# Performance work log

Measured on AMD Instinct MI355X. Metric: run time of the kernel, lower is better.

## Reference

```python
import jax, jax.numpy as jnp
import numpy as np

D_MODEL = 1024
NUM_HEADS = 16
D_K = D_MODEL // NUM_HEADS
B, S = 4, 2048


def setup_inputs() -> dict:
    key = jax.random.key(0)
    ks = jax.random.split(key, 12)
    Q = jax.random.normal(ks[0], (B, S, D_MODEL), dtype=jnp.float32)
    K = jax.random.normal(ks[1], (B, S, D_MODEL), dtype=jnp.float32)
    V = jax.random.normal(ks[2], (B, S, D_MODEL), dtype=jnp.float32)
    # causal mask: 1 where attention allowed, 0 where blocked
    mask = jnp.tril(jnp.ones((S, S), dtype=jnp.int32))[None, None, :, :]
    sc = 1.0 / np.sqrt(D_MODEL)
    Wq = jax.random.normal(ks[3], (D_MODEL, D_MODEL), dtype=jnp.float32) * sc
    Wk = jax.random.normal(ks[4], (D_MODEL, D_MODEL), dtype=jnp.float32) * sc
    Wv = jax.random.normal(ks[5], (D_MODEL, D_MODEL), dtype=jnp.float32) * sc
    Wo = jax.random.normal(ks[6], (D_MODEL, D_MODEL), dtype=jnp.float32) * sc
    bq = jnp.zeros((D_MODEL,), dtype=jnp.float32)
    bk = jnp.zeros((D_MODEL,), dtype=jnp.float32)
    bv = jnp.zeros((D_MODEL,), dtype=jnp.float32)
    bo = jnp.zeros((D_MODEL,), dtype=jnp.float32)
    return {"Q": Q, "K": K, "V": V, "mask": mask,
            "Wq": Wq, "bq": bq, "Wk": Wk, "bk": bk,
            "Wv": Wv, "bv": bv, "Wo": Wo, "bo": bo}


def reference(Q, K, V, mask, Wq, bq, Wk, bk, Wv, bv, Wo, bo):
    b = Q.shape[0]
    # projections (torch Linear: x @ W.T + b; here W stored as [in, out])
    q = Q @ Wq + bq
    k = K @ Wk + bk
    v = V @ Wv + bv
    # [B, S, D] -> [B, H, S, d_k]
    def split_heads(x):
        return x.reshape(b, -1, NUM_HEADS, D_K).transpose(0, 2, 1, 3)
    q, k, v = split_heads(q), split_heads(k), split_heads(v)
    scores = jnp.einsum('bhqd,bhkd->bhqk', q, k) / jnp.sqrt(jnp.float32(D_K))
    scores = jnp.where(mask == 0, -jnp.inf, scores)
    attn = jax.nn.softmax(scores, axis=-1)
    out = jnp.einsum('bhqk,bhkd->bhqd', attn, v)  # [B, H, S, d_k]
    out = out.transpose(0, 2, 1, 3).reshape(b, -1, NUM_HEADS * D_K)
    return out @ Wo + bo
```

## Files before the change

kernel.cpp:

```cpp
#include <hip/hip_runtime.h>

typedef __bf16 bf16_t;
typedef __bf16 bf16x8 __attribute__((ext_vector_type(8)));
typedef __bf16 bf16x4 __attribute__((ext_vector_type(4)));
typedef float  floatx4 __attribute__((ext_vector_type(4)));

#define D_MODEL 1024
#define S_LEN   2048
#define NHEAD   16
#define DK      64
#define BATCH   4
#define MROWS   (BATCH * S_LEN)
#define QSCALE  0.18033688011112042f

__device__ __forceinline__ void load_lds16(const void* gsrc, void* ldst) {
  __builtin_amdgcn_global_load_lds(
      (const __attribute__((address_space(1))) void*)gsrc,
      (__attribute__((address_space(3))) void*)ldst, 16, 0, 0);
}

__device__ __forceinline__ unsigned pack_bf16(float a, float b) {
  union { bf16_t h[2]; unsigned u; } t;
  t.h[0] = (bf16_t)a; t.h[1] = (bf16_t)b;
  return t.u;
}

__device__ __forceinline__ float bperm_f(int addr, float v) {
  union { float f; int i; } in, out;
  in.f = v;
  out.i = __builtin_amdgcn_ds_bpermute(addr, in.i);
  return out.f;
}

__global__ __launch_bounds__(256)
void transpose_w_kernel(const float* __restrict__ W0, const float* __restrict__ W1,
                        const float* __restrict__ W2, const float* __restrict__ W3,
                        bf16_t* __restrict__ T0, bf16_t* __restrict__ T1,
                        bf16_t* __restrict__ T2, bf16_t* __restrict__ T3)
{
  const int z = blockIdx.z;
  const float* W = z == 0 ? W0 : (z == 1 ? W1 : (z == 2 ? W2 : W3));
  bf16_t* Wt     = z == 0 ? T0 : (z == 1 ? T1 : (z == 2 ? T2 : T3));

  __shared__ float tile[64][65];
  const int x0 = blockIdx.x * 64;
  const int y0 = blockIdx.y * 64;
  const int tid = threadIdx.x;
  const int r = tid >> 4;
  const int c = (tid & 15) << 2;
#pragma unroll
  for (int p = 0; p < 4; p++) {
    floatx4 v = *(const floatx4*)&W[(size_t)(y0 + p * 16 + r) * D_MODEL + x0 + c];
    tile[p * 16 + r][c + 0] = v[0];
    tile[p * 16 + r][c + 1] = v[1];
    tile[p * 16 + r][c + 2] = v[2];
    tile[p * 16 + r][c + 3] = v[3];
  }
  __syncthreads();
#pragma unroll
  for (int p = 0; p < 4; p++) {
    int row = p * 16 + r;
    bf16x4 o;
    o[0] = (bf16_t)tile[c + 0][row];
    o[1] = (bf16_t)tile[c + 1][row];
    o[2] = (bf16_t)tile[c + 2][row];
    o[3] = (bf16_t)tile[c + 3][row];
    *(bf16x4*)&Wt[(size_t)(x0 + row) * D_MODEL + y0 + c] = o;
  }
}

__global__ __launch_bounds__(256, 3)
void qkv_kernel(const float* __restrict__ Qi, const float* __restrict__ Ki,
                const float* __restrict__ Vi, const bf16_t* __restrict__ Wcat,
                const float* __restrict__ bq, const float* __restrict__ bk,
                const float* __restrict__ bv,
                bf16_t* __restrict__ qo, bf16_t* __restrict__ ko,
                bf16_t* __restrict__ vo)
{
  __shared__ bf16_t As[128 * 40];
  __shared__ bf16_t Bs[128 * 32];

  const int n0g = blockIdx.x << 7;
  const int z = n0g >> 10;
  const float* A = z == 0 ? Qi : (z == 1 ? Ki : Vi);

  const int m0 = blockIdx.y << 7;
  const int tid = threadIdx.x;
  const int lane = tid & 63;
  const int w = tid >> 6;
  const int l15 = lane & 15;
  const int quad = lane >> 4;
  const int wy = (w >> 1) << 6;
  const int wx = (w & 1) << 6;
  const int w64 = w << 6;

  floatx4 acc[4][4];
#pragma unroll
  for (int i = 0; i < 4; i++)
#pragma unroll
    for (int j = 0; j < 4; j++)
#pragma unroll
      for (int r = 0; r < 4; r++) acc[i][j][r] = 0.0f;

  for (int kt = 0; kt < 32; kt++) {
    const int k0 = kt << 5;
    __syncthreads();
#pragma unroll
    for (int p = 0; p < 2; p++) {
      int slot = p * 256 + w64 + lane;
      int row = slot >> 2;
      int kc = (slot & 3) ^ (row & 3);
      load_lds16(&Wcat[(size_t)(n0g + row) * D_MODEL + k0 + (kc << 3)],
                 &Bs[(size_t)(p * 256 + w64) << 3]);
    }
#pragma unroll
    for (int p = 0; p < 4; p++) {
      int idx = p * 256 + tid;
      int r = idx >> 3, c = idx & 7;
      floatx4 v = *(const floatx4*)&A[(size_t)(m0 + r) * D_MODEL + k0 + (c << 2)];
      bf16x4 o;
      o[0] = (bf16_t)v[0]; o[1] = (bf16_t)v[1];
      o[2] = (bf16_t)v[2]; o[3] = (bf16_t)v[3];
      *(bf16x4*)&As[r * 40 + (c << 2)] = o;
    }
    __syncthreads();

    bf16x8 af[4], bfv[4];
#pragma unroll
    for (int mi = 0; mi < 4; mi++) {
      int m = wy + mi * 16 + l15;
      af[mi] = *(const bf16x8*)&As[m * 40 + (quad << 3)];
    }
#pragma unroll
    for (int ni = 0; ni < 4; ni++) {
      int n = wx + ni * 16 + l15;
      bfv[ni] = *(const bf16x8*)&Bs[n * 32 + ((quad ^ (n & 3)) << 3)];
    }
#pragma unroll
    for (int mi = 0; mi < 4; mi++)
#pragma unroll
      for (int ni = 0; ni < 4; ni++)
        acc[mi][ni] = __builtin_amdgcn_mfma_f32_16x16x32_bf16(
            af[mi], bfv[ni], acc[mi][ni], 0, 0, 0);
  }

  const float* bias = z == 0 ? bq : (z == 1 ? bk : bv);
  bf16_t* outp      = z == 0 ? qo : (z == 1 ? ko : vo);
  const float scl   = (z == 0) ? QSCALE : 1.0f;
#pragma unroll
  for (int mi = 0; mi < 4; mi++) {
#pragma unroll
    for (int ni = 0; ni < 4; ni++) {
      const int nn = (n0g + wx + ni * 16 + l15) & (D_MODEL - 1);
      const float bvv = bias[nn];
      const int h = nn >> 6, d = nn & 63;
#pragma unroll
      for (int r = 0; r < 4; r++) {
        const int m = m0 + wy + mi * 16 + quad * 4 + r;
        const int b = m >> 11, s = m & (S_LEN - 1);
        float v = (acc[mi][ni][r] + bvv) * scl;
        if (z < 2) {
          outp[((((size_t)(b * NHEAD + h) << 11) + s) << 6) + d] = (bf16_t)v;
        } else {
          outp[((((size_t)(b * NHEAD + h) << 6) + d) << 11) + s] = (bf16_t)v;
        }
      }
    }
  }
}

__global__ __launch_bounds__(256)
void out_gemm_kernel(const bf16_t* __restrict__ A, const bf16_t* __restrict__ Wt,
                     const float* __restrict__ bias, float* __restrict__ out)
{
  __shared__ bf16_t As[128 * 32];
  __shared__ bf16_t Bs[128 * 32];
  const int m0 = blockIdx.y << 7;
  const int n0 = blockIdx.x << 7;
  const int tid = threadIdx.x;
  const int lane = tid & 63;
  const int w = tid >> 6;
  const int l15 = lane & 15;
  const int quad = lane >> 4;
  const int wy = (w >> 1) << 6;
  const int wx = (w & 1) << 6;
  const int w64 = w << 6;

  floatx4 acc[4][4];
#pragma unroll
  for (int i = 0; i < 4; i++)
#pragma unroll
    for (int j = 0; j < 4; j++)
#pragma unroll
      for (int r = 0; r < 4; r++) acc[i][j][r] = 0.0f;

  for (int kt = 0; kt < 32; kt++) {
    const int k0 = kt << 5;
    __syncthreads();
#pragma unroll
    for (int p = 0; p < 2; p++) {
      int slot = p * 256 + w64 + lane;
      int row = slot >> 2;
      int kc = (slot & 3) ^ (row & 3);
      load_lds16(&A[(size_t)(m0 + row) * D_MODEL + k0 + (kc << 3)],
                 &As[(size_t)(p * 256 + w64) << 3]);
      load_lds16(&Wt[(size_t)(n0 + row) * D_MODEL + k0 + (kc << 3)],
                 &Bs[(size_t)(p * 256 + w64) << 3]);
    }
    __syncthreads();

    bf16x8 af[4], bfv[4];
#pragma unroll
    for (int mi = 0; mi < 4; mi++) {
      int m = wy + mi * 16 + l15;
      af[mi] = *(const bf16x8*)&As[m * 32 + ((quad ^ (m & 3)) << 3)];
    }
#pragma unroll
    for (int ni = 0; ni < 4; ni++) {
      int n = wx + ni * 16 + l15;
      bfv[ni] = *(const bf16x8*)&Bs[n * 32 + ((quad ^ (n & 3)) << 3)];
    }
#pragma unroll
    for (int mi = 0; mi < 4; mi++)
#pragma unroll
      for (int ni = 0; ni < 4; ni++)
        acc[mi][ni] = __builtin_amdgcn_mfma_f32_16x16x32_bf16(
            af[mi], bfv[ni], acc[mi][ni], 0, 0, 0);
  }

#pragma unroll
  for (int mi = 0; mi < 4; mi++) {
#pragma unroll
    for (int ni = 0; ni < 4; ni++) {
      const int nbase = n0 + wx + ni * 16 + l15;
      const float bv = bias[nbase];
#pragma unroll
      for (int r = 0; r < 4; r++) {
        const int m = m0 + wy + mi * 16 + quad * 4 + r;
        out[((size_t)m << 10) + nbase] = acc[mi][ni][r] + bv;
      }
    }
  }
}

__global__ __launch_bounds__(256, 4)
void attn_kernel(const bf16_t* __restrict__ qp, const bf16_t* __restrict__ kp,
                 const bf16_t* __restrict__ vtp, bf16_t* __restrict__ ob)
{
  __shared__ bf16_t Kt0[64 * 64];
  __shared__ bf16_t Kt1[64 * 64];
  __shared__ bf16_t Vt0[64 * 64];
  __shared__ bf16_t Vt1[64 * 64];

  const int pair = blockIdx.x;
  const int bh = blockIdx.y;
  const int tid = threadIdx.x;
  const int w = tid >> 6;
  const int lane = tid & 63;
  const int l15 = lane & 15;
  const int quad = lane >> 4;

  const bf16_t* Qh = qp + ((size_t)bh << 17);
  const bf16_t* Kh = kp + ((size_t)bh << 17);
  const bf16_t* Vh = vtp + ((size_t)bh << 17);
  const int b = bh >> 4, h = bh & 15;

  auto stage = [&](int k0s, bf16_t* dK, bf16_t* dV) {
#pragma unroll
    for (int p = 0; p < 2; p++) {
      const int sbase = (w << 7) + (p << 6);
      const int slot = sbase + lane;
      const int row = slot >> 3;
      const int c = (slot & 7) ^ (row & 7);
      load_lds16(&Kh[((size_t)(k0s + row) << 6) + (c << 3)], &dK[sbase << 3]);
      load_lds16(&Vh[((size_t)row << 11) + k0s + (c << 3)], &dV[sbase << 3]);
    }
  };

  int par = 0;

  auto phase = [&](int qt, bool prefetch_next_phase) {
    const int q0 = qt << 6;
    const int qbase = q0 + (w << 4);
    const int nkb = qt + 1;

    bf16x8 qf[2];
#pragma unroll
    for (int ks = 0; ks < 2; ks++)
      qf[ks] = *(const bf16x8*)&Qh[(size_t)(qbase + l15) * DK +
                                   ks * 32 + (quad << 3)];

    floatx4 acc_o[4];
    float m_i = -1e30f, l_i = 0.0f;
#pragma unroll
    for (int nd = 0; nd < 4; nd++)
#pragma unroll
      for (int r = 0; r < 4; r++) acc_o[nd][r] = 0.0f;

    for (int kb = 0; kb < nkb; kb++) {
      const int k0 = kb << 6;
      __syncthreads();

      const bf16_t* cK = par ? Kt1 : Kt0;
      const bf16_t* cV = par ? Vt1 : Vt0;
      bf16_t* nK = par ? Kt0 : Kt1;
      bf16_t* nV = par ? Vt0 : Vt1;

      if (kb + 1 < nkb)            stage((kb + 1) << 6, nK, nV);
      else if (prefetch_next_phase) stage(0, nK, nV);

      bf16x8 bk[2][4];
#pragma unroll
      for (int ks = 0; ks < 2; ks++)
#pragma unroll
        for (int ni = 0; ni < 4; ni++) {
          const int row = ni * 16 + l15;
          const int cp = ((ks << 2) + quad) ^ (row & 7);
          bk[ks][ni] = *(const bf16x8*)&cK[(row << 6) + (cp << 3)];
        }

      floatx4 st[4];
#pragma unroll
      for (int ni = 0; ni < 4; ni++)
#pragma unroll
        for (int r = 0; r < 4; r++) st[ni][r] = 0.0f;
#pragma unroll
      for (int ks = 0; ks < 2; ks++)
#pragma unroll
        for (int ni = 0; ni < 4; ni++)
          st[ni] = __builtin_amdgcn_mfma_f32_16x16x32_bf16(
              bk[ks][ni], qf[ks], st[ni], 0, 0, 0);

      if (k0 + 63 > qbase) {
        const int qrow = qbase + l15;
#pragma unroll
        for (int ni = 0; ni < 4; ni++) {
          const int keyb = k0 + ni * 16 + quad * 4;
#pragma unroll
          for (int r = 0; r < 4; r++)
            if (keyb + r > qrow) st[ni][r] = -1e30f;
        }
      }

      float v = st[0][0];
#pragma unroll
      for (int ni = 0; ni < 4; ni++)
#pragma unroll
        for (int r = 0; r < 4; r++) v = fmaxf(v, st[ni][r]);
      v = fmaxf(v, __shfl_xor(v, 16));
      v = fmaxf(v, __shfl_xor(v, 32));
      const float mn = fmaxf(m_i, v);
      const float alpha = __builtin_amdgcn_exp2f(m_i - mn);
      m_i = mn;

      unsigned pd[4][2];
      float s = 0.0f;
#pragma unroll
      for (int c = 0; c < 4; c++)
#pragma unroll
        for (int hh = 0; hh < 2; hh++) {
          float p0 = __builtin_amdgcn_exp2f(st[c][2 * hh]     - m_i);
          float p1 = __builtin_amdgcn_exp2f(st[c][2 * hh + 1] - m_i);
          s += p0 + p1;
          pd[c][hh] = pack_bf16(p0, p1);
        }
      s += __shfl_xor(s, 16);
      s += __shfl_xor(s, 32);
      l_i = l_i * alpha + s;

#pragma unroll
      for (int r = 0; r < 4; r++) {
        float ab = bperm_f((quad * 4 + r) << 2, alpha);
#pragma unroll
        for (int nd = 0; nd < 4; nd++) acc_o[nd][r] *= ab;
      }

      union AV { unsigned u[4]; bf16x8 v; };
      AV av[2];
#pragma unroll
      for (int ks = 0; ks < 2; ks++)
#pragma unroll
        for (int i = 0; i < 4; i++) {
          const int addr = ((((2 * quad + (i >> 1)) & 3) << 4) | l15) << 2;
          int lo = __builtin_amdgcn_ds_bpermute(addr, (int)pd[ks * 2][i & 1]);
          int hi = __builtin_amdgcn_ds_bpermute(addr, (int)pd[ks * 2 + 1][i & 1]);
          av[ks].u[i] = (unsigned)(quad >= 2 ? hi : lo);
        }

#pragma unroll
      for (int ks = 0; ks < 2; ks++) {
        bf16x8 bvv[4];
#pragma unroll
        for (int nd = 0; nd < 4; nd++) {
          const int row = nd * 16 + l15;
          const int cp = ((ks << 2) + quad) ^ (row & 7);
          bvv[nd] = *(const bf16x8*)&cV[(row << 6) + (cp << 3)];
        }
#pragma unroll
        for (int nd = 0; nd < 4; nd++)
          acc_o[nd] = __builtin_amdgcn_mfma_f32_16x16x32_bf16(
              av[ks].v, bvv[nd], acc_o[nd], 0, 0, 0);
      }

      par ^= 1;
    }

    const float inv = 1.0f / l_i;
#pragma unroll
    for (int r = 0; r < 4; r++) {
      const float linv = bperm_f((quad * 4 + r) << 2, inv);
      const int sRow = qbase + quad * 4 + r;
#pragma unroll
      for (int nd = 0; nd < 4; nd++) {
        const int d = nd * 16 + l15;
        ob[(((size_t)(b * S_LEN + sRow)) << 10) + h * 64 + d] =
            (bf16_t)(acc_o[nd][r] * linv);
      }
    }
  };

  stage(0, Kt0, Vt0);
  phase(31 - pair, true);
  phase(pair, false);
}

extern "C" void kernel_launch(void* const* d_in, const int* in_sizes, int n_in,
                              void* d_out, int out_size, void* d_ws, size_t ws_size,
                              hipStream_t stream)
{
  (void)in_sizes; (void)n_in; (void)out_size; (void)ws_size;
  const float* Q  = (const float*)d_in[0];
  const float* K  = (const float*)d_in[1];
  const float* V  = (const float*)d_in[2];
  const float* Wq = (const float*)d_in[4];
  const float* bq = (const float*)d_in[5];
  const float* Wk = (const float*)d_in[6];
  const float* bk = (const float*)d_in[7];
  const float* Wv = (const float*)d_in[8];
  const float* bv = (const float*)d_in[9];
  const float* Wo = (const float*)d_in[10];
  const float* bo = (const float*)d_in[11];
  float* out = (float*)d_out;

  const size_t NELT = (size_t)MROWS * D_MODEL;
  bf16_t* qp   = (bf16_t*)d_ws;
  bf16_t* kp   = qp + NELT;
  bf16_t* vtp  = kp + NELT;
  bf16_t* obuf = vtp + NELT;
  bf16_t* wqt  = obuf + NELT;
  bf16_t* wkt  = wqt + (size_t)D_MODEL * D_MODEL;
  bf16_t* wvt  = wkt + (size_t)D_MODEL * D_MODEL;
  bf16_t* wot  = wvt + (size_t)D_MODEL * D_MODEL;

  dim3 blk(256);
  transpose_w_kernel<<<dim3(16, 16, 4), blk, 0, stream>>>(
      Wq, Wk, Wv, Wo, wqt, wkt, wvt, wot);

  qkv_kernel<<<dim3(3 * D_MODEL / 128, MROWS / 128), blk, 0, stream>>>(
      Q, K, V, wqt, bq, bk, bv, qp, kp, vtp);

  attn_kernel<<<dim3(16, BATCH * NHEAD), blk, 0, stream>>>(qp, kp, vtp, obuf);

  out_gemm_kernel<<<dim3(D_MODEL / 128, MROWS / 128), blk, 0, stream>>>(
      obuf, wot, bo, out);
}
```

Baseline: 387.8 us.

## Load fp32 activations via direct-to-LDS DMA and swizzle block order for L2 reuse

```diff
diff --git a/kernel.cpp b/kernel.cpp
--- a/kernel.cpp
+++ b/kernel.cpp
@@ -77,14 +77,18 @@
                 bf16_t* __restrict__ qo, bf16_t* __restrict__ ko,
                 bf16_t* __restrict__ vo)
 {
-  __shared__ bf16_t As[128 * 40];
+  __shared__ float  Asf[128 * 32];
   __shared__ bf16_t Bs[128 * 32];
 
-  const int n0g = blockIdx.x << 7;
-  const int z = n0g >> 10;
+  const int L = blockIdx.x + 24 * blockIdx.y;
+  const int j = (L >> 3) & 7;
+  const int s = ((L >> 6) << 3) | (L & 7);
+  const int z = s >> 6;
+  const int n0g = (((z << 3) | j)) << 7;
+  const int m0 = (s & 63) << 7;
+
   const float* A = z == 0 ? Qi : (z == 1 ? Ki : Vi);
 
-  const int m0 = blockIdx.y << 7;
   const int tid = threadIdx.x;
   const int lane = tid & 63;
   const int w = tid >> 6;
@@ -98,9 +102,9 @@
 #pragma unroll
   for (int i = 0; i < 4; i++)
 #pragma unroll
-    for (int j = 0; j < 4; j++)
-#pragma unroll
-      for (int r = 0; r < 4; r++) acc[i][j][r] = 0.0f;
+    for (int jj = 0; jj < 4; jj++)
+#pragma unroll
+      for (int r = 0; r < 4; r++) acc[i][jj][r] = 0.0f;
 
   for (int kt = 0; kt < 32; kt++) {
     const int k0 = kt << 5;
@@ -115,21 +119,28 @@
     }
 #pragma unroll
     for (int p = 0; p < 4; p++) {
-      int idx = p * 256 + tid;
-      int r = idx >> 3, c = idx & 7;
-      floatx4 v = *(const floatx4*)&A[(size_t)(m0 + r) * D_MODEL + k0 + (c << 2)];
-      bf16x4 o;
-      o[0] = (bf16_t)v[0]; o[1] = (bf16_t)v[1];
-      o[2] = (bf16_t)v[2]; o[3] = (bf16_t)v[3];
-      *(bf16x4*)&As[r * 40 + (c << 2)] = o;
+      int sbase = (w << 8) + (p << 6);
+      int slot = sbase + lane;
+      int row = slot >> 3;
+      int ca = (slot & 7) ^ (row & 7);
+      load_lds16(&A[(size_t)(m0 + row) * D_MODEL + k0 + (ca << 2)],
+                 &Asf[(size_t)sbase << 2]);
     }
     __syncthreads();
 
     bf16x8 af[4], bfv[4];
 #pragma unroll
     for (int mi = 0; mi < 4; mi++) {
-      int m = wy + mi * 16 + l15;
-      af[mi] = *(const bf16x8*)&As[m * 40 + (quad << 3)];
+      const int m = wy + mi * 16 + l15;
+      const int e = m & 7;
+      floatx4 f0 = *(const floatx4*)&Asf[(m << 5) + ((((quad << 1))     ^ e) << 2)];
+      floatx4 f1 = *(const floatx4*)&Asf[(m << 5) + ((((quad << 1) | 1) ^ e) << 2)];
+      bf16x8 o;
+      o[0] = (bf16_t)f0[0]; o[1] = (bf16_t)f0[1];
+      o[2] = (bf16_t)f0[2]; o[3] = (bf16_t)f0[3];
+      o[4] = (bf16_t)f1[0]; o[5] = (bf16_t)f1[1];
+      o[6] = (bf16_t)f1[2]; o[7] = (bf16_t)f1[3];
+      af[mi] = o;
     }
 #pragma unroll
     for (int ni = 0; ni < 4; ni++) {
@@ -157,12 +168,12 @@
 #pragma unroll
       for (int r = 0; r < 4; r++) {
         const int m = m0 + wy + mi * 16 + quad * 4 + r;
-        const int b = m >> 11, s = m & (S_LEN - 1);
+        const int b = m >> 11, srow = m & (S_LEN - 1);
         float v = (acc[mi][ni][r] + bvv) * scl;
         if (z < 2) {
-          outp[((((size_t)(b * NHEAD + h) << 11) + s) << 6) + d] = (bf16_t)v;
+          outp[((((size_t)(b * NHEAD + h) << 11) + srow) << 6) + d] = (bf16_t)v;
         } else {
-          outp[((((size_t)(b * NHEAD + h) << 6) + d) << 11) + s] = (bf16_t)v;
+          outp[((((size_t)(b * NHEAD + h) << 6) + d) << 11) + srow] = (bf16_t)v;
         }
       }
     }
@@ -175,8 +186,9 @@
 {
   __shared__ bf16_t As[128 * 32];
   __shared__ bf16_t Bs[128 * 32];
-  const int m0 = blockIdx.y << 7;
-  const int n0 = blockIdx.x << 7;
+  const int L = blockIdx.x + 8 * blockIdx.y;
+  const int n0 = (((L >> 3) & 7)) << 7;
+  const int m0 = ((((L >> 6) << 3) | (L & 7))) << 7;
   const int tid = threadIdx.x;
   const int lane = tid & 63;
   const int w = tid >> 6;
@@ -190,9 +202,9 @@
 #pragma unroll
   for (int i = 0; i < 4; i++)
 #pragma unroll
-    for (int j = 0; j < 4; j++)
-#pragma unroll
-      for (int r = 0; r < 4; r++) acc[i][j][r] = 0.0f;
+    for (int jj = 0; jj < 4; jj++)
+#pragma unroll
+      for (int r = 0; r < 4; r++) acc[i][jj][r] = 0.0f;
 
   for (int kt = 0; kt < 32; kt++) {
     const int k0 = kt << 5;
@@ -306,7 +318,7 @@
       bf16_t* nK = par ? Kt0 : Kt1;
       bf16_t* nV = par ? Vt0 : Vt1;
 
-      if (kb + 1 < nkb)            stage((kb + 1) << 6, nK, nV);
+      if (kb + 1 < nkb)             stage((kb + 1) << 6, nK, nV);
       else if (prefetch_next_phase) stage(0, nK, nV);
 
       bf16x8 bk[2][4];
@@ -354,19 +366,19 @@
       m_i = mn;
 
       unsigned pd[4][2];
-      float s = 0.0f;
+      float ssum = 0.0f;
 #pragma unroll
       for (int c = 0; c < 4; c++)
 #pragma unroll
         for (int hh = 0; hh < 2; hh++) {
           float p0 = __builtin_amdgcn_exp2f(st[c][2 * hh]     - m_i);
           float p1 = __builtin_amdgcn_exp2f(st[c][2 * hh + 1] - m_i);
-          s += p0 + p1;
+          ssum += p0 + p1;
           pd[c][hh] = pack_bf16(p0, p1);
         }
-      s += __shfl_xor(s, 16);
-      s += __shfl_xor(s, 32);
-      l_i = l_i * alpha + s;
+      ssum += __shfl_xor(ssum, 16);
+      ssum += __shfl_xor(ssum, 32);
+      l_i = l_i * alpha + ssum;
 
 #pragma unroll
       for (int r = 0; r < 4; r++) {
```

Measured after the change: 372.1 us. 4.1% less time.
